# Kernel tuning notes

Hardware: AMD Instinct MI355X
Metric: run time of the kernel (lower is better)

The kernel has to match this reference:

```python
import jax, jax.numpy as jnp
import numpy as np

HID = 256

def setup_inputs() -> dict:
    key = jax.random.key(0)
    ks = jax.random.split(key, 16)
    B, N, DIN, DOUT = 256, 1024, 64, 128
    def lin(k, fin, fout):
        kw, kb = jax.random.split(k)
        s = 1.0 / np.sqrt(fin)
        W = jax.random.uniform(kw, (fin, fout), jnp.float32, -s, s)
        b = jax.random.uniform(kb, (fout,), jnp.float32, -s, s)
        return W, b
    x = jax.random.normal(ks[0], (B, N, DIN), jnp.float32)
    mask = jax.random.randint(ks[1], (B, N), 0, 2) > 0
    pw1, pb1 = lin(ks[2], DIN, HID)
    pw2, pb2 = lin(ks[3], HID, HID)
    pw3, pb3 = lin(ks[4], HID, HID)
    rw1, rb1 = lin(ks[5], HID, HID)
    rw2, rb2 = lin(ks[6], HID, HID)
    rw3, rb3 = lin(ks[7], HID, DOUT)
    return dict(x=x, mask=mask, pw1=pw1, pb1=pb1, pw2=pw2, pb2=pb2, pw3=pw3, pb3=pb3,
                rw1=rw1, rb1=rb1, rw2=rw2, rb2=rb2, rw3=rw3, rb3=rb3)

def reference(x, mask, pw1, pb1, pw2, pb2, pw3, pb3, rw1, rb1, rw2, rb2, rw3, rb3):
    # x: [B, N, din], mask: [B, N] bool
    # phi per element (padding elements are zeroed before the pool, matching
    # the torch pack/pad pipeline which only runs phi on valid elements)
    h = jax.nn.relu(jnp.einsum('bnd,dh->bnh', x, pw1) + pb1)
    h = jax.nn.relu(jnp.einsum('bnh,hk->bnk', h, pw2) + pb2)
    h = jnp.einsum('bnh,hk->bnk', h, pw3) + pb3
    m = mask.astype(x.dtype)[..., None]                  # [B, N, 1]
    pooled = jnp.sum(h * m, axis=1)                      # [B, 256]
    o = jax.nn.relu(pooled @ rw1 + rb1)
    o = jax.nn.relu(o @ rw2 + rb2)
    o = o @ rw3 + rb3                                    # [B, dout]
    # rows with zero valid elements get exactly 0 (torch leaves res at 0.0)
    valid = jnp.any(mask, axis=1, keepdims=True)
    return jnp.where(valid, o, jnp.zeros((), dtype=o.dtype))
```

## Files before the change

kernel.cpp:

```cpp
#include <hip/hip_runtime.h>

namespace {
constexpr int NB = 256, NN = 1024, DIN = 64, HID = 256, DOUT = 128;
constexpr int MT = 64;

typedef __attribute__((ext_vector_type(8))) short bf16x8;
typedef __attribute__((ext_vector_type(4))) float f32x4;

constexpr size_t PW1_OFF = 0;
constexpr size_t PW2_OFF = (size_t)DIN * HID * 2;

__device__ inline unsigned short f2bf(float f) {
    union { float f; unsigned u; } v; v.f = f;
    unsigned r = v.u + 0x7FFF + ((v.u >> 16) & 1);
    return (unsigned short)(r >> 16);
}

__global__ void prep(const float* __restrict__ pw1, const float* __restrict__ pw2,
                     unsigned short* __restrict__ w1p, unsigned short* __restrict__ w2p) {
    int i = blockIdx.x * 256 + threadIdx.x;
    if (i < DIN * HID / 8) {
        int s0 = i * 8;
        int k = s0 >> 8, n0 = s0 & 255;
        float4 v0 = *(const float4*)(pw1 + s0);
        float4 v1 = *(const float4*)(pw1 + s0 + 4);
        float vv[8] = {v0.x, v0.y, v0.z, v0.w, v1.x, v1.y, v1.z, v1.w};
        int j = k & 7, quad = (k >> 3) & 3, kk = k >> 5;
#pragma unroll
        for (int e = 0; e < 8; ++e) {
            int n = n0 + e, strip = n >> 4, l15 = n & 15;
            w1p[strip * 1024 + kk * 512 + (quad * 16 + l15) * 8 + j] = f2bf(vv[e]);
        }
    }
    if (i < HID * HID / 8) {
        int s0 = i * 8;
        int k = s0 >> 8, n0 = s0 & 255;
        float4 v0 = *(const float4*)(pw2 + s0);
        float4 v1 = *(const float4*)(pw2 + s0 + 4);
        float vv[8] = {v0.x, v0.y, v0.z, v0.w, v1.x, v1.y, v1.z, v1.w};
        int j = k & 7, quad = (k >> 3) & 3, kk = k >> 5;
#pragma unroll
        for (int e = 0; e < 8; ++e) {
            int n = n0 + e, strip = n >> 4, l15 = n & 15;
            w2p[strip * 4096 + kk * 512 + (quad * 16 + l15) * 8 + j] = f2bf(vv[e]);
        }
    }
}

__device__ inline float4 dotseg(const float* __restrict__ buf, const float* __restrict__ W,
                                int c, int s) {
    const float4* W4 = (const float4*)W;
    float4 acc = make_float4(0.f, 0.f, 0.f, 0.f);
#pragma unroll 8
    for (int i = 0; i < 32; ++i) {
        int k = s * 32 + i;
        float bk = buf[k];
        float4 w = W4[(size_t)k * 64 + c];
        acc.x = fmaf(bk, w.x, acc.x);
        acc.y = fmaf(bk, w.y, acc.y);
        acc.z = fmaf(bk, w.z, acc.z);
        acc.w = fmaf(bk, w.w, acc.w);
    }
    return acc;
}

__launch_bounds__(512, 2)
__global__ void deepset(const float* __restrict__ x, const int* __restrict__ mask,
                        const float* __restrict__ pb1, const float* __restrict__ pb2,
                        const unsigned short* __restrict__ w1p,
                        const unsigned short* __restrict__ w2p,
                        const float* __restrict__ pw3, const float* __restrict__ pb3,
                        const float* __restrict__ rw1, const float* __restrict__ rb1,
                        const float* __restrict__ rw2, const float* __restrict__ rb2,
                        const float* __restrict__ rw3, const float* __restrict__ rb3,
                        float* __restrict__ out)
{
    __shared__ unsigned short xs[2][MT * 64];
    __shared__ unsigned short h1s[MT * 256];
    __shared__ short vlist[NN];
    __shared__ float pooledS[HID];
    __shared__ float part[8][HID];
    __shared__ float bufB[HID], bufC[HID];
    __shared__ int cnt_s;

    const int b = blockIdx.x, t = threadIdx.x;
    const int lane = t & 63, wq = t >> 6;
    const int quad = lane >> 4, l15 = lane & 15;

    if (t == 0) cnt_s = 0;
    __syncthreads();
    if (mask[b * NN + t] != 0)       { int i = atomicAdd(&cnt_s, 1); vlist[i] = (short)t; }
    if (mask[b * NN + t + 512] != 0) { int i = atomicAdd(&cnt_s, 1); vlist[i] = (short)(t + 512); }
    __syncthreads();
    const int cnt = cnt_s;

    const uint4* w1q = (const uint4*)w1p;
    const uint4* w2q = (const uint4*)w2p;
    uint4 w1f[2][2], w2f[8][2];
#pragma unroll
    for (int j = 0; j < 2; ++j) {
        int strip = wq * 2 + j;
#pragma unroll
        for (int kk = 0; kk < 2; ++kk) w1f[kk][j] = w1q[(strip * 2 + kk) * 64 + lane];
#pragma unroll
        for (int kk = 0; kk < 8; ++kk) w2f[kk][j] = w2q[(strip * 8 + kk) * 64 + lane];
    }
    float bias1[2], bias2[2];
#pragma unroll
    for (int j = 0; j < 2; ++j) {
        int c = wq * 32 + j * 16 + l15;
        bias1[j] = pb1[c]; bias2[j] = pb2[c];
    }

    float pool[2] = {0.f, 0.f};
    const float* xb = x + (size_t)b * NN * DIN;
    const int gr = t >> 3, seg8 = t & 7;
    const int xoff = gr * 64 + ((seg8 ^ (gr & 7)) << 3);

    {
        float4 a0 = make_float4(0.f,0.f,0.f,0.f), a1 = a0;
        if (gr < min(MT, cnt)) {
            const float4* p = (const float4*)(xb + (size_t)vlist[gr] * DIN + seg8 * 8);
            a0 = p[0]; a1 = p[1];
        }
        unsigned short tmp[8] = {f2bf(a0.x),f2bf(a0.y),f2bf(a0.z),f2bf(a0.w),
                                 f2bf(a1.x),f2bf(a1.y),f2bf(a1.z),f2bf(a1.w)};
        *(uint4*)&xs[0][xoff] = *(const uint4*)tmp;
    }

    int cur = 0;
    for (int base = 0; base < cnt; base += MT) {
        __syncthreads();

        f32x4 acc[4][2];
#pragma unroll
        for (int f = 0; f < 4; ++f)
#pragma unroll
            for (int j = 0; j < 2; ++j) acc[f][j] = (f32x4){0.f,0.f,0.f,0.f};
#pragma unroll
        for (int kk = 0; kk < 2; ++kk) {
            bf16x8 a[4];
#pragma unroll
            for (int f = 0; f < 4; ++f)
                a[f] = *(const bf16x8*)&xs[cur][(f*16 + l15)*64 + (((kk*4 + quad) ^ (l15 & 7)) << 3)];
#pragma unroll
            for (int j = 0; j < 2; ++j) {
                bf16x8 bw = __builtin_bit_cast(bf16x8, w1f[kk][j]);
#pragma unroll
                for (int f = 0; f < 4; ++f)
                    acc[f][j] = __builtin_amdgcn_mfma_f32_16x16x32_bf16(a[f], bw, acc[f][j], 0, 0, 0);
            }
        }
#pragma unroll
        for (int f = 0; f < 4; ++f)
#pragma unroll
            for (int j = 0; j < 2; ++j) {
                int col = wq * 32 + j * 16 + l15, kb = col >> 3, cl = col & 7;
#pragma unroll
                for (int r = 0; r < 4; ++r) {
                    int row = f * 16 + quad * 4 + r;
                    float h = fmaxf(acc[f][j][r] + bias1[j], 0.f);
                    h1s[row * 256 + ((kb ^ (row & 7)) << 3) + cl] = f2bf(h);
                }
            }

        float4 n0 = make_float4(0.f,0.f,0.f,0.f), n1 = n0;
        const bool hn = (base + MT) < cnt;
        if (hn && gr < cnt - (base + MT)) {
            const float4* p = (const float4*)(xb + (size_t)vlist[base + MT + gr] * DIN + seg8 * 8);
            n0 = p[0]; n1 = p[1];
        }
        __syncthreads();

        f32x4 acc2[4][2];
#pragma unroll
        for (int f = 0; f < 4; ++f)
#pragma unroll
            for (int j = 0; j < 2; ++j) acc2[f][j] = (f32x4){0.f,0.f,0.f,0.f};
#pragma unroll
        for (int kk = 0; kk < 8; ++kk) {
            bf16x8 a[4];
#pragma unroll
            for (int f = 0; f < 4; ++f)
                a[f] = *(const bf16x8*)&h1s[(f*16 + l15)*256 + (((kk*4 + quad) ^ (l15 & 7)) << 3)];
#pragma unroll
            for (int j = 0; j < 2; ++j) {
                bf16x8 bw = __builtin_bit_cast(bf16x8, w2f[kk][j]);
#pragma unroll
                for (int f = 0; f < 4; ++f)
                    acc2[f][j] = __builtin_amdgcn_mfma_f32_16x16x32_bf16(a[f], bw, acc2[f][j], 0, 0, 0);
            }
        }
#pragma unroll
        for (int f = 0; f < 4; ++f)
#pragma unroll
            for (int r = 0; r < 4; ++r) {
                bool v = (base + f * 16 + quad * 4 + r) < cnt;
#pragma unroll
                for (int j = 0; j < 2; ++j) {
                    float h = fmaxf(acc2[f][j][r] + bias2[j], 0.f);
                    pool[j] += v ? h : 0.f;
                }
            }

        if (hn) {
            unsigned short tmp[8] = {f2bf(n0.x),f2bf(n0.y),f2bf(n0.z),f2bf(n0.w),
                                     f2bf(n1.x),f2bf(n1.y),f2bf(n1.z),f2bf(n1.w)};
            *(uint4*)&xs[cur ^ 1][xoff] = *(const uint4*)tmp;
        }
        cur ^= 1;
    }

#pragma unroll
    for (int j = 0; j < 2; ++j) {
        float v = pool[j];
        v += __shfl_xor(v, 16, 64);
        v += __shfl_xor(v, 32, 64);
        if (quad == 0) pooledS[wq * 32 + j * 16 + l15] = v;
    }
    __syncthreads();

    const int c = t & 63, s = t >> 6;
    {
        float4 p = dotseg(pooledS, pw3, c, s);
        ((float4*)part[s])[c] = p;
        __syncthreads();
        if (t < HID) {
            float v = (float)cnt * pb3[t];
#pragma unroll
            for (int g = 0; g < 8; ++g) v += part[g][t];
            bufB[t] = v;
        }
        __syncthreads();
    }
    {
        float4 p = dotseg(bufB, rw1, c, s);
        ((float4*)part[s])[c] = p;
        __syncthreads();
        if (t < HID) {
            float v = rb1[t];
#pragma unroll
            for (int g = 0; g < 8; ++g) v += part[g][t];
            bufC[t] = fmaxf(v, 0.f);
        }
        __syncthreads();
    }
    {
        float4 p = dotseg(bufC, rw2, c, s);
        ((float4*)part[s])[c] = p;
        __syncthreads();
        if (t < HID) {
            float v = rb2[t];
#pragma unroll
            for (int g = 0; g < 8; ++g) v += part[g][t];
            bufB[t] = fmaxf(v, 0.f);
        }
        __syncthreads();
    }
    {
        const int c4 = t & 31, s4 = t >> 5;
        const float4* W4 = (const float4*)rw3;
        float4 acc = make_float4(0.f, 0.f, 0.f, 0.f);
#pragma unroll 8
        for (int i = 0; i < 16; ++i) {
            int k = s4 * 16 + i;
            float bk = bufB[k];
            float4 w = W4[(size_t)k * 32 + c4];
            acc.x = fmaf(bk, w.x, acc.x);
            acc.y = fmaf(bk, w.y, acc.y);
            acc.z = fmaf(bk, w.z, acc.z);
            acc.w = fmaf(bk, w.w, acc.w);
        }
        float* part2 = &part[0][0];
        ((float4*)(part2 + s4 * DOUT))[c4] = acc;
        __syncthreads();
        if (t < DOUT) {
            float v = rb3[t];
#pragma unroll
            for (int g = 0; g < 16; ++g) v += part2[g * DOUT + t];
            out[b * DOUT + t] = (cnt > 0) ? v : 0.f;
        }
    }
}
}

extern "C" void kernel_launch(void* const* d_in, const int* in_sizes, int n_in,
                              void* d_out, int out_size, void* d_ws, size_t ws_size,
                              hipStream_t stream) {
    const float* x    = (const float*)d_in[0];
    const int*   mask = (const int*)  d_in[1];
    const float* pw1  = (const float*)d_in[2];
    const float* pb1  = (const float*)d_in[3];
    const float* pw2  = (const float*)d_in[4];
    const float* pb2  = (const float*)d_in[5];
    const float* pw3  = (const float*)d_in[6];
    const float* pb3  = (const float*)d_in[7];
    const float* rw1  = (const float*)d_in[8];
    const float* rb1  = (const float*)d_in[9];
    const float* rw2  = (const float*)d_in[10];
    const float* rb2  = (const float*)d_in[11];
    const float* rw3  = (const float*)d_in[12];
    const float* rb3  = (const float*)d_in[13];
    float* out = (float*)d_out;

    unsigned short* w1p = (unsigned short*)((char*)d_ws + PW1_OFF);
    unsigned short* w2p = (unsigned short*)((char*)d_ws + PW2_OFF);

    prep<<<dim3(32), dim3(256), 0, stream>>>(pw1, pw2, w1p, w2p);
    deepset<<<dim3(NB), dim3(512), 0, stream>>>(x, mask, pb1, pb2, w1p, w2p,
                                                pw3, pb3, rw1, rb1, rw2, rb2, rw3, rb3, out);
}
```

Baseline: 146.0 us.

## Split phi across two blocks per batch row and move rho to separate kernel

The fused kernel is split in two. phi_half runs two blocks per batch row, each taking half the set elements with a 32-row tile and higher occupancy, and writes partial pooled sums and counts to workspace. rho_k then sums the partials and runs the rho MLP, with two batch rows per block. The change also compacts the mask with a ballot, swaps the MFMA operand order so outputs are written as packed bf16 stores, and raises MFMA priority with setprio. The aim is to put more blocks on the GPU and shorten each block's serial work, at the cost of an extra launch and a workspace round trip.

```diff
diff --git a/kernel.cpp b/kernel.cpp
--- a/kernel.cpp
+++ b/kernel.cpp
@@ -2,13 +2,16 @@
 
 namespace {
 constexpr int NB = 256, NN = 1024, DIN = 64, HID = 256, DOUT = 128;
-constexpr int MT = 64;
+constexpr int MT = 32;
+constexpr int NH = 512;
 
 typedef __attribute__((ext_vector_type(8))) short bf16x8;
 typedef __attribute__((ext_vector_type(4))) float f32x4;
 
-constexpr size_t PW1_OFF = 0;
-constexpr size_t PW2_OFF = (size_t)DIN * HID * 2;
+constexpr size_t PW1_OFF  = 0;
+constexpr size_t PW2_OFF  = (size_t)DIN * HID * 2;
+constexpr size_t POOL_OFF = PW2_OFF + (size_t)HID * HID * 2;
+constexpr size_t CNT_OFF  = POOL_OFF + (size_t)2 * NB * HID * 4;
 
 __device__ inline unsigned short f2bf(float f) {
     union { float f; unsigned u; } v; v.f = f;
@@ -47,15 +50,192 @@
     }
 }
 
-__device__ inline float4 dotseg(const float* __restrict__ buf, const float* __restrict__ W,
-                                int c, int s) {
+__launch_bounds__(512, 4)
+__global__ void phi_half(const float* __restrict__ x, const int* __restrict__ mask,
+                         const float* __restrict__ pb1, const float* __restrict__ pb2,
+                         const unsigned short* __restrict__ w1p,
+                         const unsigned short* __restrict__ w2p,
+                         float* __restrict__ pool_part, int* __restrict__ cnt_part)
+{
+    __shared__ unsigned short xs[2][MT * 64];
+    __shared__ unsigned short h1s[MT * 256];
+    __shared__ short vlist[NH];
+    __shared__ int cnt_s;
+
+    const int bid = blockIdx.x;
+    const int b = bid >> 1, half = bid & 1;
+    const int t = threadIdx.x;
+    const int lane = t & 63, wq = t >> 6;
+    const int quad = lane >> 4, l15 = lane & 15;
+
+    if (t == 0) cnt_s = 0;
+    __syncthreads();
+    {
+        int m = mask[b * NN + half * NH + t] != 0;
+        unsigned long long bal = __ballot(m);
+        int pos = __popcll(bal & ((1ULL << lane) - 1ULL));
+        int wbase = 0;
+        if (lane == 0) wbase = atomicAdd(&cnt_s, (int)__popcll(bal));
+        wbase = __shfl(wbase, 0, 64);
+        if (m) vlist[wbase + pos] = (short)t;
+    }
+    __syncthreads();
+    const int cnt = cnt_s;
+
+    const uint4* w1q = (const uint4*)w1p;
+    const uint4* w2q = (const uint4*)w2p;
+    uint4 w1f[2][2], w2f[8][2];
+#pragma unroll
+    for (int j = 0; j < 2; ++j) {
+        int strip = wq * 2 + j;
+#pragma unroll
+        for (int kk = 0; kk < 2; ++kk) w1f[kk][j] = w1q[(strip * 2 + kk) * 64 + lane];
+#pragma unroll
+        for (int kk = 0; kk < 8; ++kk) w2f[kk][j] = w2q[(strip * 8 + kk) * 64 + lane];
+    }
+
+    const float* xb = x + ((size_t)b * NN + (size_t)half * NH) * DIN;
+    const int gr = t >> 4, s16 = t & 15;
+    const int xoff = gr * 64 + (((s16 >> 1) ^ (gr & 7)) << 3) + ((s16 & 1) << 2);
+
+    {
+        float4 a0 = make_float4(0.f, 0.f, 0.f, 0.f);
+        if (gr < min(MT, cnt))
+            a0 = *(const float4*)(xb + (size_t)vlist[gr] * DIN + s16 * 4);
+        unsigned lo = (unsigned)f2bf(a0.x) | ((unsigned)f2bf(a0.y) << 16);
+        unsigned hi = (unsigned)f2bf(a0.z) | ((unsigned)f2bf(a0.w) << 16);
+        *(uint2*)&xs[0][xoff] = make_uint2(lo, hi);
+    }
+
+    float pool[2][4] = {{0.f, 0.f, 0.f, 0.f}, {0.f, 0.f, 0.f, 0.f}};
+    const int cb0 = wq * 32 + quad * 4;
+    const int sw = l15 & 7;
+    int cur = 0;
+
+    for (int base = 0; base < cnt; base += MT) {
+        __syncthreads();
+
+        f32x4 acc[2][2];
+#pragma unroll
+        for (int j = 0; j < 2; ++j)
+#pragma unroll
+            for (int f = 0; f < 2; ++f) acc[j][f] = (f32x4){0.f, 0.f, 0.f, 0.f};
+        __builtin_amdgcn_s_setprio(1);
+#pragma unroll
+        for (int kk = 0; kk < 2; ++kk) {
+            bf16x8 a[2];
+#pragma unroll
+            for (int f = 0; f < 2; ++f)
+                a[f] = *(const bf16x8*)&xs[cur][(f * 16 + l15) * 64 + (((kk * 4 + quad) ^ sw) << 3)];
+#pragma unroll
+            for (int j = 0; j < 2; ++j) {
+                bf16x8 bw = __builtin_bit_cast(bf16x8, w1f[kk][j]);
+#pragma unroll
+                for (int f = 0; f < 2; ++f)
+                    acc[j][f] = __builtin_amdgcn_mfma_f32_16x16x32_bf16(bw, a[f], acc[j][f], 0, 0, 0);
+            }
+        }
+        __builtin_amdgcn_s_setprio(0);
+
+#pragma unroll
+        for (int j = 0; j < 2; ++j) {
+            float4 b1 = *(const float4*)&pb1[cb0 + j * 16];
+            int kb = wq * 4 + j * 2 + (quad >> 1);
+#pragma unroll
+            for (int f = 0; f < 2; ++f) {
+                int row = f * 16 + l15;
+                unsigned lo = (unsigned)f2bf(fmaxf(acc[j][f][0] + b1.x, 0.f))
+                            | ((unsigned)f2bf(fmaxf(acc[j][f][1] + b1.y, 0.f)) << 16);
+                unsigned hi = (unsigned)f2bf(fmaxf(acc[j][f][2] + b1.z, 0.f))
+                            | ((unsigned)f2bf(fmaxf(acc[j][f][3] + b1.w, 0.f)) << 16);
+                *(uint2*)&h1s[row * 256 + ((kb ^ sw) << 3) + ((quad & 1) << 2)] = make_uint2(lo, hi);
+            }
+        }
+
+        float4 n0 = make_float4(0.f, 0.f, 0.f, 0.f);
+        const bool hn = (base + MT) < cnt;
+        if (hn && gr < cnt - (base + MT))
+            n0 = *(const float4*)(xb + (size_t)vlist[base + MT + gr] * DIN + s16 * 4);
+
+        __syncthreads();
+
+        f32x4 acc2[2][2];
+#pragma unroll
+        for (int j = 0; j < 2; ++j)
+#pragma unroll
+            for (int f = 0; f < 2; ++f) acc2[j][f] = (f32x4){0.f, 0.f, 0.f, 0.f};
+        __builtin_amdgcn_s_setprio(1);
+#pragma unroll
+        for (int kk = 0; kk < 8; ++kk) {
+            bf16x8 a[2];
+#pragma unroll
+            for (int f = 0; f < 2; ++f)
+                a[f] = *(const bf16x8*)&h1s[(f * 16 + l15) * 256 + (((kk * 4 + quad) ^ sw) << 3)];
+#pragma unroll
+            for (int j = 0; j < 2; ++j) {
+                bf16x8 bw = __builtin_bit_cast(bf16x8, w2f[kk][j]);
+#pragma unroll
+                for (int f = 0; f < 2; ++f)
+                    acc2[j][f] = __builtin_amdgcn_mfma_f32_16x16x32_bf16(bw, a[f], acc2[j][f], 0, 0, 0);
+            }
+        }
+        __builtin_amdgcn_s_setprio(0);
+
+#pragma unroll
+        for (int j = 0; j < 2; ++j) {
+            float4 b2 = *(const float4*)&pb2[cb0 + j * 16];
+#pragma unroll
+            for (int f = 0; f < 2; ++f) {
+                bool vf = (base + f * 16 + l15) < cnt;
+                float h0 = fmaxf(acc2[j][f][0] + b2.x, 0.f);
+                float h1 = fmaxf(acc2[j][f][1] + b2.y, 0.f);
+                float h2 = fmaxf(acc2[j][f][2] + b2.z, 0.f);
+                float h3 = fmaxf(acc2[j][f][3] + b2.w, 0.f);
+                pool[j][0] += vf ? h0 : 0.f;
+                pool[j][1] += vf ? h1 : 0.f;
+                pool[j][2] += vf ? h2 : 0.f;
+                pool[j][3] += vf ? h3 : 0.f;
+            }
+        }
+
+        if (hn) {
+            unsigned lo = (unsigned)f2bf(n0.x) | ((unsigned)f2bf(n0.y) << 16);
+            unsigned hi = (unsigned)f2bf(n0.z) | ((unsigned)f2bf(n0.w) << 16);
+            *(uint2*)&xs[cur ^ 1][xoff] = make_uint2(lo, hi);
+        }
+        cur ^= 1;
+    }
+
+#pragma unroll
+    for (int j = 0; j < 2; ++j)
+#pragma unroll
+        for (int r = 0; r < 4; ++r) {
+            float v = pool[j][r];
+            v += __shfl_xor(v, 1, 64);
+            v += __shfl_xor(v, 2, 64);
+            v += __shfl_xor(v, 4, 64);
+            v += __shfl_xor(v, 8, 64);
+            pool[j][r] = v;
+        }
+    if (l15 == 0) {
+#pragma unroll
+        for (int j = 0; j < 2; ++j) {
+            float4 pv = make_float4(pool[j][0], pool[j][1], pool[j][2], pool[j][3]);
+            *(float4*)&pool_part[(size_t)bid * HID + cb0 + j * 16] = pv;
+        }
+    }
+    if (t == 0) cnt_part[bid] = cnt;
+}
+
+__device__ inline float4 gemvseg(const float* __restrict__ buf, const float* __restrict__ W,
+                                 int c, int s, int nseg, int strid4) {
     const float4* W4 = (const float4*)W;
     float4 acc = make_float4(0.f, 0.f, 0.f, 0.f);
 #pragma unroll 8
-    for (int i = 0; i < 32; ++i) {
-        int k = s * 32 + i;
+    for (int i = 0; i < nseg; ++i) {
+        int k = s * nseg + i;
         float bk = buf[k];
-        float4 w = W4[(size_t)k * 64 + c];
+        float4 w = W4[(size_t)k * strid4 + c];
         acc.x = fmaf(bk, w.x, acc.x);
         acc.y = fmaf(bk, w.y, acc.y);
         acc.z = fmaf(bk, w.z, acc.z);
@@ -64,221 +244,68 @@
     return acc;
 }
 
-__launch_bounds__(512, 2)
-__global__ void deepset(const float* __restrict__ x, const int* __restrict__ mask,
-                        const float* __restrict__ pb1, const float* __restrict__ pb2,
-                        const unsigned short* __restrict__ w1p,
-                        const unsigned short* __restrict__ w2p,
-                        const float* __restrict__ pw3, const float* __restrict__ pb3,
-                        const float* __restrict__ rw1, const float* __restrict__ rb1,
-                        const float* __restrict__ rw2, const float* __restrict__ rb2,
-                        const float* __restrict__ rw3, const float* __restrict__ rb3,
-                        float* __restrict__ out)
+__launch_bounds__(512)
+__global__ void rho_k(const float* __restrict__ pool_part, const int* __restrict__ cnt_part,
+                      const float* __restrict__ pw3, const float* __restrict__ pb3,
+                      const float* __restrict__ rw1, const float* __restrict__ rb1,
+                      const float* __restrict__ rw2, const float* __restrict__ rb2,
+                      const float* __restrict__ rw3, const float* __restrict__ rb3,
+                      float* __restrict__ out)
 {
-    __shared__ unsigned short xs[2][MT * 64];
-    __shared__ unsigned short h1s[MT * 256];
-    __shared__ short vlist[NN];
-    __shared__ float pooledS[HID];
-    __shared__ float part[8][HID];
-    __shared__ float bufB[HID], bufC[HID];
-    __shared__ int cnt_s;
-
-    const int b = blockIdx.x, t = threadIdx.x;
-    const int lane = t & 63, wq = t >> 6;
-    const int quad = lane >> 4, l15 = lane & 15;
-
-    if (t == 0) cnt_s = 0;
+    __shared__ float bufA[2][HID], bufB[2][HID];
+    __shared__ float part[2][4][HID];
+    __shared__ int cnts[2];
+    const int t = threadIdx.x;
+    const int g = t >> 8, gt = t & 255;
+    const int b = blockIdx.x * 2 + g;
+
+    if (gt == 0) cnts[g] = cnt_part[2 * b] + cnt_part[2 * b + 1];
+    bufA[g][gt] = pool_part[(size_t)(2 * b) * HID + gt]
+                + pool_part[(size_t)(2 * b + 1) * HID + gt];
     __syncthreads();
-    if (mask[b * NN + t] != 0)       { int i = atomicAdd(&cnt_s, 1); vlist[i] = (short)t; }
-    if (mask[b * NN + t + 512] != 0) { int i = atomicAdd(&cnt_s, 1); vlist[i] = (short)(t + 512); }
-    __syncthreads();
-    const int cnt = cnt_s;
-
-    const uint4* w1q = (const uint4*)w1p;
-    const uint4* w2q = (const uint4*)w2p;
-    uint4 w1f[2][2], w2f[8][2];
-#pragma unroll
-    for (int j = 0; j < 2; ++j) {
-        int strip = wq * 2 + j;
-#pragma unroll
-        for (int kk = 0; kk < 2; ++kk) w1f[kk][j] = w1q[(strip * 2 + kk) * 64 + lane];
-#pragma unroll
-        for (int kk = 0; kk < 8; ++kk) w2f[kk][j] = w2q[(strip * 8 + kk) * 64 + lane];
-    }
-    float bias1[2], bias2[2];
-#pragma unroll
-    for (int j = 0; j < 2; ++j) {
-        int c = wq * 32 + j * 16 + l15;
-        bias1[j] = pb1[c]; bias2[j] = pb2[c];
-    }
-
-    float pool[2] = {0.f, 0.f};
-    const float* xb = x + (size_t)b * NN * DIN;
-    const int gr = t >> 3, seg8 = t & 7;
-    const int xoff = gr * 64 + ((seg8 ^ (gr & 7)) << 3);
-
-    {
-        float4 a0 = make_float4(0.f,0.f,0.f,0.f), a1 = a0;
-        if (gr < min(MT, cnt)) {
-            const float4* p = (const float4*)(xb + (size_t)vlist[gr] * DIN + seg8 * 8);
-            a0 = p[0]; a1 = p[1];
-        }
-        unsigned short tmp[8] = {f2bf(a0.x),f2bf(a0.y),f2bf(a0.z),f2bf(a0.w),
-                                 f2bf(a1.x),f2bf(a1.y),f2bf(a1.z),f2bf(a1.w)};
-        *(uint4*)&xs[0][xoff] = *(const uint4*)tmp;
-    }
-
-    int cur = 0;
-    for (int base = 0; base < cnt; base += MT) {
-        __syncthreads();
-
-        f32x4 acc[4][2];
-#pragma unroll
-        for (int f = 0; f < 4; ++f)
-#pragma unroll
-            for (int j = 0; j < 2; ++j) acc[f][j] = (f32x4){0.f,0.f,0.f,0.f};
-#pragma unroll
-        for (int kk = 0; kk < 2; ++kk) {
-            bf16x8 a[4];
-#pragma unroll
-            for (int f = 0; f < 4; ++f)
-                a[f] = *(const bf16x8*)&xs[cur][(f*16 + l15)*64 + (((kk*4 + quad) ^ (l15 & 7)) << 3)];
-#pragma unroll
-            for (int j = 0; j < 2; ++j) {
-                bf16x8 bw = __builtin_bit_cast(bf16x8, w1f[kk][j]);
-#pragma unroll
-                for (int f = 0; f < 4; ++f)
-                    acc[f][j] = __builtin_amdgcn_mfma_f32_16x16x32_bf16(a[f], bw, acc[f][j], 0, 0, 0);
-            }
-        }
-#pragma unroll
-        for (int f = 0; f < 4; ++f)
-#pragma unroll
-            for (int j = 0; j < 2; ++j) {
-                int col = wq * 32 + j * 16 + l15, kb = col >> 3, cl = col & 7;
-#pragma unroll
-                for (int r = 0; r < 4; ++r) {
-                    int row = f * 16 + quad * 4 + r;
-                    float h = fmaxf(acc[f][j][r] + bias1[j], 0.f);
-                    h1s[row * 256 + ((kb ^ (row & 7)) << 3) + cl] = f2bf(h);
-                }
-            }
-
-        float4 n0 = make_float4(0.f,0.f,0.f,0.f), n1 = n0;
-        const bool hn = (base + MT) < cnt;
-        if (hn && gr < cnt - (base + MT)) {
-            const float4* p = (const float4*)(xb + (size_t)vlist[base + MT + gr] * DIN + seg8 * 8);
-            n0 = p[0]; n1 = p[1];
-        }
-        __syncthreads();
-
-        f32x4 acc2[4][2];
-#pragma unroll
-        for (int f = 0; f < 4; ++f)
-#pragma unroll
-            for (int j = 0; j < 2; ++j) acc2[f][j] = (f32x4){0.f,0.f,0.f,0.f};
-#pragma unroll
-        for (int kk = 0; kk < 8; ++kk) {
-            bf16x8 a[4];
-#pragma unroll
-            for (int f = 0; f < 4; ++f)
-                a[f] = *(const bf16x8*)&h1s[(f*16 + l15)*256 + (((kk*4 + quad) ^ (l15 & 7)) << 3)];
-#pragma unroll
-            for (int j = 0; j < 2; ++j) {
-                bf16x8 bw = __builtin_bit_cast(bf16x8, w2f[kk][j]);
-#pragma unroll
-                for (int f = 0; f < 4; ++f)
-                    acc2[f][j] = __builtin_amdgcn_mfma_f32_16x16x32_bf16(a[f], bw, acc2[f][j], 0, 0, 0);
-            }
-        }
-#pragma unroll
-        for (int f = 0; f < 4; ++f)
-#pragma unroll
-            for (int r = 0; r < 4; ++r) {
-                bool v = (base + f * 16 + quad * 4 + r) < cnt;
-#pragma unroll
-                for (int j = 0; j < 2; ++j) {
-                    float h = fmaxf(acc2[f][j][r] + bias2[j], 0.f);
-                    pool[j] += v ? h : 0.f;
-                }
-            }
-
-        if (hn) {
-            unsigned short tmp[8] = {f2bf(n0.x),f2bf(n0.y),f2bf(n0.z),f2bf(n0.w),
-                                     f2bf(n1.x),f2bf(n1.y),f2bf(n1.z),f2bf(n1.w)};
-            *(uint4*)&xs[cur ^ 1][xoff] = *(const uint4*)tmp;
-        }
-        cur ^= 1;
-    }
-
-#pragma unroll
-    for (int j = 0; j < 2; ++j) {
-        float v = pool[j];
-        v += __shfl_xor(v, 16, 64);
-        v += __shfl_xor(v, 32, 64);
-        if (quad == 0) pooledS[wq * 32 + j * 16 + l15] = v;
-    }
-    __syncthreads();
-
-    const int c = t & 63, s = t >> 6;
-    {
-        float4 p = dotseg(pooledS, pw3, c, s);
-        ((float4*)part[s])[c] = p;
-        __syncthreads();
-        if (t < HID) {
-            float v = (float)cnt * pb3[t];
-#pragma unroll
-            for (int g = 0; g < 8; ++g) v += part[g][t];
-            bufB[t] = v;
-        }
-        __syncthreads();
-    }
-    {
-        float4 p = dotseg(bufB, rw1, c, s);
-        ((float4*)part[s])[c] = p;
-        __syncthreads();
-        if (t < HID) {
-            float v = rb1[t];
-#pragma unroll
-            for (int g = 0; g < 8; ++g) v += part[g][t];
-            bufC[t] = fmaxf(v, 0.f);
-        }
-        __syncthreads();
-    }
-    {
-        float4 p = dotseg(bufC, rw2, c, s);
-        ((float4*)part[s])[c] = p;
-        __syncthreads();
-        if (t < HID) {
-            float v = rb2[t];
-#pragma unroll
-            for (int g = 0; g < 8; ++g) v += part[g][t];
-            bufB[t] = fmaxf(v, 0.f);
-        }
-        __syncthreads();
-    }
-    {
-        const int c4 = t & 31, s4 = t >> 5;
-        const float4* W4 = (const float4*)rw3;
-        float4 acc = make_float4(0.f, 0.f, 0.f, 0.f);
-#pragma unroll 8
-        for (int i = 0; i < 16; ++i) {
-            int k = s4 * 16 + i;
-            float bk = bufB[k];
-            float4 w = W4[(size_t)k * 32 + c4];
-            acc.x = fmaf(bk, w.x, acc.x);
-            acc.y = fmaf(bk, w.y, acc.y);
-            acc.z = fmaf(bk, w.z, acc.z);
-            acc.w = fmaf(bk, w.w, acc.w);
-        }
-        float* part2 = &part[0][0];
-        ((float4*)(part2 + s4 * DOUT))[c4] = acc;
-        __syncthreads();
-        if (t < DOUT) {
-            float v = rb3[t];
-#pragma unroll
-            for (int g = 0; g < 16; ++g) v += part2[g * DOUT + t];
-            out[b * DOUT + t] = (cnt > 0) ? v : 0.f;
+
+    const int c = gt & 63, s = gt >> 6;
+    {
+        float4 p = gemvseg(bufA[g], pw3, c, s, 64, 64);
+        ((float4*)part[g][s])[c] = p;
+        __syncthreads();
+        float v = (float)cnts[g] * pb3[gt];
+#pragma unroll
+        for (int q = 0; q < 4; ++q) v += part[g][q][gt];
+        bufB[g][gt] = v;
+        __syncthreads();
+    }
+    {
+        float4 p = gemvseg(bufB[g], rw1, c, s, 64, 64);
+        ((float4*)part[g][s])[c] = p;
+        __syncthreads();
+        float v = rb1[gt];
+#pragma unroll
+        for (int q = 0; q < 4; ++q) v += part[g][q][gt];
+        bufA[g][gt] = fmaxf(v, 0.f);
+        __syncthreads();
+    }
+    {
+        float4 p = gemvseg(bufA[g], rw2, c, s, 64, 64);
+        ((float4*)part[g][s])[c] = p;
+        __syncthreads();
+        float v = rb2[gt];
+#pragma unroll
+        for (int q = 0; q < 4; ++q) v += part[g][q][gt];
+        bufB[g][gt] = fmaxf(v, 0.f);
+        __syncthreads();
+    }
+    {
+        const int c4 = gt & 31, s4 = gt >> 5;
+        float4 p = gemvseg(bufB[g], rw3, c4, s4, 32, 32);
+        float* pf = &part[g][0][0];
+        ((float4*)(pf + s4 * DOUT))[c4] = p;
+        __syncthreads();
+        if (gt < DOUT) {
+            float v = rb3[gt];
+#pragma unroll
+            for (int q = 0; q < 8; ++q) v += pf[q * DOUT + gt];
+            out[(size_t)b * DOUT + gt] = (cnts[g] > 0) ? v : 0.f;
         }
     }
 }
@@ -305,8 +332,12 @@
 
     unsigned short* w1p = (unsigned short*)((char*)d_ws + PW1_OFF);
     unsigned short* w2p = (unsigned short*)((char*)d_ws + PW2_OFF);
+    float* pool_part = (float*)((char*)d_ws + POOL_OFF);
+    int* cnt_part = (int*)((char*)d_ws + CNT_OFF);
 
     prep<<<dim3(32), dim3(256), 0, stream>>>(pw1, pw2, w1p, w2p);
-    deepset<<<dim3(NB), dim3(512), 0, stream>>>(x, mask, pb1, pb2, w1p, w2p,
-                                                pw3, pb3, rw1, rb1, rw2, rb2, rw3, rb3, out);
-}
+    phi_half<<<dim3(NB * 2), dim3(512), 0, stream>>>(x, mask, pb1, pb2, w1p, w2p,
+                                                     pool_part, cnt_part);
+    rho_k<<<dim3(NB / 2), dim3(512), 0, stream>>>(pool_part, cnt_part, pw3, pb3,
+                                                  rw1, rb1, rw2, rb2, rw3, rb3, out);
+}
```

Result: slower. 188.9 us (+29.4%).

## Split each batch row across two 512-thread halves in a 1024-thread block

Applied to the files above, without the earlier changes.

Each block now runs 1024 threads, and each half processes its own 512-element slice of the set with its own xs and h1s buffers. The two partial pools are summed before the rho MLP, and that MLP is split over 16 or 32 segments. Compaction now uses a wave ballot plus one atomic per wave instead of per-element atomics. The aim is to halve the serial phi loop per block and raise per-CU parallelism, at the cost of running both halves to the longer half's count and losing the two-blocks-per-CU occupancy.

```diff
diff --git a/kernel.cpp b/kernel.cpp
--- a/kernel.cpp
+++ b/kernel.cpp
@@ -3,12 +3,13 @@
 namespace {
 constexpr int NB = 256, NN = 1024, DIN = 64, HID = 256, DOUT = 128;
 constexpr int MT = 64;
+constexpr int NH2 = 512;
 
 typedef __attribute__((ext_vector_type(8))) short bf16x8;
 typedef __attribute__((ext_vector_type(4))) float f32x4;
 
-constexpr size_t PW1_OFF = 0;
-constexpr size_t PW2_OFF = (size_t)DIN * HID * 2;
+constexpr size_t PW1_OFF  = 0;
+constexpr size_t PW2_OFF  = (size_t)DIN * HID * 2;
 
 __device__ inline unsigned short f2bf(float f) {
     union { float f; unsigned u; } v; v.f = f;
@@ -47,13 +48,13 @@
     }
 }
 
-__device__ inline float4 dotseg(const float* __restrict__ buf, const float* __restrict__ W,
-                                int c, int s) {
+__device__ inline float4 dotseg16(const float* __restrict__ buf, const float* __restrict__ W,
+                                  int c, int s) {
     const float4* W4 = (const float4*)W;
     float4 acc = make_float4(0.f, 0.f, 0.f, 0.f);
 #pragma unroll 8
-    for (int i = 0; i < 32; ++i) {
-        int k = s * 32 + i;
+    for (int i = 0; i < 16; ++i) {
+        int k = s * 16 + i;
         float bk = buf[k];
         float4 w = W4[(size_t)k * 64 + c];
         acc.x = fmaf(bk, w.x, acc.x);
@@ -64,35 +65,45 @@
     return acc;
 }
 
-__launch_bounds__(512, 2)
-__global__ void deepset(const float* __restrict__ x, const int* __restrict__ mask,
-                        const float* __restrict__ pb1, const float* __restrict__ pb2,
-                        const unsigned short* __restrict__ w1p,
-                        const unsigned short* __restrict__ w2p,
-                        const float* __restrict__ pw3, const float* __restrict__ pb3,
-                        const float* __restrict__ rw1, const float* __restrict__ rb1,
-                        const float* __restrict__ rw2, const float* __restrict__ rb2,
-                        const float* __restrict__ rw3, const float* __restrict__ rb3,
-                        float* __restrict__ out)
+__launch_bounds__(1024, 1)
+__global__ void deepset_fused(const float* __restrict__ x, const int* __restrict__ mask,
+                              const float* __restrict__ pb1, const float* __restrict__ pb2,
+                              const unsigned short* __restrict__ w1p,
+                              const unsigned short* __restrict__ w2p,
+                              const float* __restrict__ pw3, const float* __restrict__ pb3,
+                              const float* __restrict__ rw1, const float* __restrict__ rb1,
+                              const float* __restrict__ rw2, const float* __restrict__ rb2,
+                              const float* __restrict__ rw3, const float* __restrict__ rb3,
+                              float* __restrict__ out)
 {
-    __shared__ unsigned short xs[2][MT * 64];
-    __shared__ unsigned short h1s[MT * 256];
-    __shared__ short vlist[NN];
-    __shared__ float pooledS[HID];
-    __shared__ float part[8][HID];
+    __shared__ unsigned short xs[2][2][MT * 64];
+    __shared__ unsigned short h1s[2][MT * 256];
+    __shared__ short vlist[2][NH2];
+    __shared__ float poolH[2][HID];
+    __shared__ float part[16][HID];
     __shared__ float bufB[HID], bufC[HID];
-    __shared__ int cnt_s;
-
-    const int b = blockIdx.x, t = threadIdx.x;
-    const int lane = t & 63, wq = t >> 6;
+    __shared__ int cnt_sh[2];
+
+    const int b = blockIdx.x;
+    const int t = threadIdx.x;
+    const int hh = t >> 9, u = t & 511;
+    const int lane = u & 63, wq = u >> 6;
     const int quad = lane >> 4, l15 = lane & 15;
 
-    if (t == 0) cnt_s = 0;
+    if (t < 2) cnt_sh[t] = 0;
     __syncthreads();
-    if (mask[b * NN + t] != 0)       { int i = atomicAdd(&cnt_s, 1); vlist[i] = (short)t; }
-    if (mask[b * NN + t + 512] != 0) { int i = atomicAdd(&cnt_s, 1); vlist[i] = (short)(t + 512); }
+    {
+        int m = mask[b * NN + hh * NH2 + u] != 0;
+        unsigned long long bal = __ballot(m);
+        int pos = __popcll(bal & ((1ULL << lane) - 1ULL));
+        int wbase = 0;
+        if (lane == 0) wbase = atomicAdd(&cnt_sh[hh], (int)__popcll(bal));
+        wbase = __shfl(wbase, 0, 64);
+        if (m) vlist[hh][wbase + pos] = (short)u;
+    }
     __syncthreads();
-    const int cnt = cnt_s;
+    const int cnt = cnt_sh[hh];
+    const int mx = max(cnt_sh[0], cnt_sh[1]);
 
     const uint4* w1q = (const uint4*)w1p;
     const uint4* w2q = (const uint4*)w2p;
@@ -113,23 +124,23 @@
     }
 
     float pool[2] = {0.f, 0.f};
-    const float* xb = x + (size_t)b * NN * DIN;
-    const int gr = t >> 3, seg8 = t & 7;
+    const float* xb = x + ((size_t)b * NN + (size_t)hh * NH2) * DIN;
+    const int gr = u >> 3, seg8 = u & 7;
     const int xoff = gr * 64 + ((seg8 ^ (gr & 7)) << 3);
 
     {
         float4 a0 = make_float4(0.f,0.f,0.f,0.f), a1 = a0;
         if (gr < min(MT, cnt)) {
-            const float4* p = (const float4*)(xb + (size_t)vlist[gr] * DIN + seg8 * 8);
+            const float4* p = (const float4*)(xb + (size_t)vlist[hh][gr] * DIN + seg8 * 8);
             a0 = p[0]; a1 = p[1];
         }
         unsigned short tmp[8] = {f2bf(a0.x),f2bf(a0.y),f2bf(a0.z),f2bf(a0.w),
                                  f2bf(a1.x),f2bf(a1.y),f2bf(a1.z),f2bf(a1.w)};
-        *(uint4*)&xs[0][xoff] = *(const uint4*)tmp;
+        *(uint4*)&xs[hh][0][xoff] = *(const uint4*)tmp;
     }
 
     int cur = 0;
-    for (int base = 0; base < cnt; base += MT) {
+    for (int base = 0; base < mx; base += MT) {
         __syncthreads();
 
         f32x4 acc[4][2];
@@ -142,7 +153,7 @@
             bf16x8 a[4];
 #pragma unroll
             for (int f = 0; f < 4; ++f)
-                a[f] = *(const bf16x8*)&xs[cur][(f*16 + l15)*64 + (((kk*4 + quad) ^ (l15 & 7)) << 3)];
+                a[f] = *(const bf16x8*)&xs[hh][cur][(f*16 + l15)*64 + (((kk*4 + quad) ^ (l15 & 7)) << 3)];
 #pragma unroll
             for (int j = 0; j < 2; ++j) {
                 bf16x8 bw = __builtin_bit_cast(bf16x8, w1f[kk][j]);
@@ -160,14 +171,14 @@
                 for (int r = 0; r < 4; ++r) {
                     int row = f * 16 + quad * 4 + r;
                     float h = fmaxf(acc[f][j][r] + bias1[j], 0.f);
-                    h1s[row * 256 + ((kb ^ (row & 7)) << 3) + cl] = f2bf(h);
+                    h1s[hh][row * 256 + ((kb ^ (row & 7)) << 3) + cl] = f2bf(h);
                 }
             }
 
         float4 n0 = make_float4(0.f,0.f,0.f,0.f), n1 = n0;
-        const bool hn = (base + MT) < cnt;
-        if (hn && gr < cnt - (base + MT)) {
-            const float4* p = (const float4*)(xb + (size_t)vlist[base + MT + gr] * DIN + seg8 * 8);
+        const bool hstore = (base + MT) < mx;
+        if (gr < cnt - (base + MT)) {
+            const float4* p = (const float4*)(xb + (size_t)vlist[hh][base + MT + gr] * DIN + seg8 * 8);
             n0 = p[0]; n1 = p[1];
         }
         __syncthreads();
@@ -182,7 +193,7 @@
             bf16x8 a[4];
 #pragma unroll
             for (int f = 0; f < 4; ++f)
-                a[f] = *(const bf16x8*)&h1s[(f*16 + l15)*256 + (((kk*4 + quad) ^ (l15 & 7)) << 3)];
+                a[f] = *(const bf16x8*)&h1s[hh][(f*16 + l15)*256 + (((kk*4 + quad) ^ (l15 & 7)) << 3)];
 #pragma unroll
             for (int j = 0; j < 2; ++j) {
                 bf16x8 bw = __builtin_bit_cast(bf16x8, w2f[kk][j]);
@@ -203,10 +214,10 @@
                 }
             }
 
-        if (hn) {
+        if (hstore) {
             unsigned short tmp[8] = {f2bf(n0.x),f2bf(n0.y),f2bf(n0.z),f2bf(n0.w),
                                      f2bf(n1.x),f2bf(n1.y),f2bf(n1.z),f2bf(n1.w)};
-            *(uint4*)&xs[cur ^ 1][xoff] = *(const uint4*)tmp;
+            *(uint4*)&xs[hh][cur ^ 1][xoff] = *(const uint4*)tmp;
         }
         cur ^= 1;
     }
@@ -216,43 +227,47 @@
         float v = pool[j];
         v += __shfl_xor(v, 16, 64);
         v += __shfl_xor(v, 32, 64);
-        if (quad == 0) pooledS[wq * 32 + j * 16 + l15] = v;
+        if (quad == 0) poolH[hh][wq * 32 + j * 16 + l15] = v;
     }
     __syncthreads();
 
+    const int ctot = cnt_sh[0] + cnt_sh[1];
+    if (t < HID) bufC[t] = poolH[0][t] + poolH[1][t];
+    __syncthreads();
+
     const int c = t & 63, s = t >> 6;
     {
-        float4 p = dotseg(pooledS, pw3, c, s);
+        float4 p = dotseg16(bufC, pw3, c, s);
         ((float4*)part[s])[c] = p;
         __syncthreads();
         if (t < HID) {
-            float v = (float)cnt * pb3[t];
-#pragma unroll
-            for (int g = 0; g < 8; ++g) v += part[g][t];
+            float v = (float)ctot * pb3[t];
+#pragma unroll
+            for (int g = 0; g < 16; ++g) v += part[g][t];
             bufB[t] = v;
         }
         __syncthreads();
     }
     {
-        float4 p = dotseg(bufB, rw1, c, s);
+        float4 p = dotseg16(bufB, rw1, c, s);
         ((float4*)part[s])[c] = p;
         __syncthreads();
         if (t < HID) {
             float v = rb1[t];
 #pragma unroll
-            for (int g = 0; g < 8; ++g) v += part[g][t];
+            for (int g = 0; g < 16; ++g) v += part[g][t];
             bufC[t] = fmaxf(v, 0.f);
         }
         __syncthreads();
     }
     {
-        float4 p = dotseg(bufC, rw2, c, s);
+        float4 p = dotseg16(bufC, rw2, c, s);
         ((float4*)part[s])[c] = p;
         __syncthreads();
         if (t < HID) {
             float v = rb2[t];
 #pragma unroll
-            for (int g = 0; g < 8; ++g) v += part[g][t];
+            for (int g = 0; g < 16; ++g) v += part[g][t];
             bufB[t] = fmaxf(v, 0.f);
         }
         __syncthreads();
@@ -262,8 +277,8 @@
         const float4* W4 = (const float4*)rw3;
         float4 acc = make_float4(0.f, 0.f, 0.f, 0.f);
 #pragma unroll 8
-        for (int i = 0; i < 16; ++i) {
-            int k = s4 * 16 + i;
+        for (int i = 0; i < 8; ++i) {
+            int k = s4 * 8 + i;
             float bk = bufB[k];
             float4 w = W4[(size_t)k * 32 + c4];
             acc.x = fmaf(bk, w.x, acc.x);
@@ -277,8 +292,8 @@
         if (t < DOUT) {
             float v = rb3[t];
 #pragma unroll
-            for (int g = 0; g < 16; ++g) v += part2[g * DOUT + t];
-            out[b * DOUT + t] = (cnt > 0) ? v : 0.f;
+            for (int g = 0; g < 32; ++g) v += part2[g * DOUT + t];
+            out[b * DOUT + t] = (ctot > 0) ? v : 0.f;
         }
     }
 }
@@ -307,6 +322,7 @@
     unsigned short* w2p = (unsigned short*)((char*)d_ws + PW2_OFF);
 
     prep<<<dim3(32), dim3(256), 0, stream>>>(pw1, pw2, w1p, w2p);
-    deepset<<<dim3(NB), dim3(512), 0, stream>>>(x, mask, pb1, pb2, w1p, w2p,
-                                                pw3, pb3, rw1, rb1, rw2, rb2, rw3, rb3, out);
-}
+    deepset_fused<<<dim3(NB), dim3(1024), 0, stream>>>(x, mask, pb1, pb2, w1p, w2p,
+                                                       pw3, pb3, rw1, rb1, rw2, rb2, rw3, rb3,
+                                                       out);
+}
```

After: 227.8 us. +56.0%, slower.

## Fuse weight prep into main kernel and software-pipeline layer1/layer2 across tiles

Applied to the files above, without the earlier changes.

Drops the separate prep kernel launch. Each block now loads pw1/pw2 directly with strided fp32 reads and converts them to bf16 fragments in registers. The tile loop is skewed so each iteration computes layer 1 for the next tile and layer 2 for the previous one, using a double-buffered h1 tile in shared memory, which halves the barriers per tile. Mask compaction uses a wave ballot with one atomic per wave. The costs are redundant uncoalesced weight loads in every block, twice the LDS for h1, and launch bounds relaxed to one block per CU, which may reduce occupancy.

```diff
diff --git a/kernel.cpp b/kernel.cpp
--- a/kernel.cpp
+++ b/kernel.cpp
@@ -6,45 +6,11 @@
 
 typedef __attribute__((ext_vector_type(8))) short bf16x8;
 typedef __attribute__((ext_vector_type(4))) float f32x4;
-
-constexpr size_t PW1_OFF = 0;
-constexpr size_t PW2_OFF = (size_t)DIN * HID * 2;
 
 __device__ inline unsigned short f2bf(float f) {
     union { float f; unsigned u; } v; v.f = f;
     unsigned r = v.u + 0x7FFF + ((v.u >> 16) & 1);
     return (unsigned short)(r >> 16);
-}
-
-__global__ void prep(const float* __restrict__ pw1, const float* __restrict__ pw2,
-                     unsigned short* __restrict__ w1p, unsigned short* __restrict__ w2p) {
-    int i = blockIdx.x * 256 + threadIdx.x;
-    if (i < DIN * HID / 8) {
-        int s0 = i * 8;
-        int k = s0 >> 8, n0 = s0 & 255;
-        float4 v0 = *(const float4*)(pw1 + s0);
-        float4 v1 = *(const float4*)(pw1 + s0 + 4);
-        float vv[8] = {v0.x, v0.y, v0.z, v0.w, v1.x, v1.y, v1.z, v1.w};
-        int j = k & 7, quad = (k >> 3) & 3, kk = k >> 5;
-#pragma unroll
-        for (int e = 0; e < 8; ++e) {
-            int n = n0 + e, strip = n >> 4, l15 = n & 15;
-            w1p[strip * 1024 + kk * 512 + (quad * 16 + l15) * 8 + j] = f2bf(vv[e]);
-        }
-    }
-    if (i < HID * HID / 8) {
-        int s0 = i * 8;
-        int k = s0 >> 8, n0 = s0 & 255;
-        float4 v0 = *(const float4*)(pw2 + s0);
-        float4 v1 = *(const float4*)(pw2 + s0 + 4);
-        float vv[8] = {v0.x, v0.y, v0.z, v0.w, v1.x, v1.y, v1.z, v1.w};
-        int j = k & 7, quad = (k >> 3) & 3, kk = k >> 5;
-#pragma unroll
-        for (int e = 0; e < 8; ++e) {
-            int n = n0 + e, strip = n >> 4, l15 = n & 15;
-            w2p[strip * 4096 + kk * 512 + (quad * 16 + l15) * 8 + j] = f2bf(vv[e]);
-        }
-    }
 }
 
 __device__ inline float4 dotseg(const float* __restrict__ buf, const float* __restrict__ W,
@@ -64,11 +30,10 @@
     return acc;
 }
 
-__launch_bounds__(512, 2)
+__launch_bounds__(512, 1)
 __global__ void deepset(const float* __restrict__ x, const int* __restrict__ mask,
-                        const float* __restrict__ pb1, const float* __restrict__ pb2,
-                        const unsigned short* __restrict__ w1p,
-                        const unsigned short* __restrict__ w2p,
+                        const float* __restrict__ pw1, const float* __restrict__ pb1,
+                        const float* __restrict__ pw2, const float* __restrict__ pb2,
                         const float* __restrict__ pw3, const float* __restrict__ pb3,
                         const float* __restrict__ rw1, const float* __restrict__ rb1,
                         const float* __restrict__ rw2, const float* __restrict__ rb2,
@@ -76,7 +41,7 @@
                         float* __restrict__ out)
 {
     __shared__ unsigned short xs[2][MT * 64];
-    __shared__ unsigned short h1s[MT * 256];
+    __shared__ unsigned short h1s[2][MT * 256];
     __shared__ short vlist[NN];
     __shared__ float pooledS[HID];
     __shared__ float part[8][HID];
@@ -89,35 +54,52 @@
 
     if (t == 0) cnt_s = 0;
     __syncthreads();
-    if (mask[b * NN + t] != 0)       { int i = atomicAdd(&cnt_s, 1); vlist[i] = (short)t; }
-    if (mask[b * NN + t + 512] != 0) { int i = atomicAdd(&cnt_s, 1); vlist[i] = (short)(t + 512); }
+#pragma unroll
+    for (int h = 0; h < 2; ++h) {
+        int idx = h * 512 + t;
+        int m = mask[b * NN + idx] != 0;
+        unsigned long long bal = __ballot(m);
+        int pos = __popcll(bal & ((1ULL << lane) - 1ULL));
+        int wbase = 0;
+        if (lane == 0) wbase = atomicAdd(&cnt_s, (int)__popcll(bal));
+        wbase = __shfl(wbase, 0, 64);
+        if (m) vlist[wbase + pos] = (short)idx;
+    }
+
+    uint4 w1f[2][2], w2f[8][2];
+    float bias1[2], bias2[2];
+#pragma unroll
+    for (int j = 0; j < 2; ++j) {
+        const int col = wq * 32 + j * 16 + l15;
+        bias1[j] = pb1[col]; bias2[j] = pb2[col];
+#pragma unroll
+        for (int kk = 0; kk < 2; ++kk) {
+            unsigned short tmp[8];
+#pragma unroll
+            for (int jj = 0; jj < 8; ++jj)
+                tmp[jj] = f2bf(pw1[(size_t)(kk * 32 + quad * 8 + jj) * HID + col]);
+            w1f[kk][j] = *(const uint4*)tmp;
+        }
+#pragma unroll
+        for (int kk = 0; kk < 8; ++kk) {
+            unsigned short tmp[8];
+#pragma unroll
+            for (int jj = 0; jj < 8; ++jj)
+                tmp[jj] = f2bf(pw2[(size_t)(kk * 32 + quad * 8 + jj) * HID + col]);
+            w2f[kk][j] = *(const uint4*)tmp;
+        }
+    }
+
     __syncthreads();
     const int cnt = cnt_s;
-
-    const uint4* w1q = (const uint4*)w1p;
-    const uint4* w2q = (const uint4*)w2p;
-    uint4 w1f[2][2], w2f[8][2];
-#pragma unroll
-    for (int j = 0; j < 2; ++j) {
-        int strip = wq * 2 + j;
-#pragma unroll
-        for (int kk = 0; kk < 2; ++kk) w1f[kk][j] = w1q[(strip * 2 + kk) * 64 + lane];
-#pragma unroll
-        for (int kk = 0; kk < 8; ++kk) w2f[kk][j] = w2q[(strip * 8 + kk) * 64 + lane];
-    }
-    float bias1[2], bias2[2];
-#pragma unroll
-    for (int j = 0; j < 2; ++j) {
-        int c = wq * 32 + j * 16 + l15;
-        bias1[j] = pb1[c]; bias2[j] = pb2[c];
-    }
+    const int T = (cnt + MT - 1) / MT;
 
     float pool[2] = {0.f, 0.f};
     const float* xb = x + (size_t)b * NN * DIN;
     const int gr = t >> 3, seg8 = t & 7;
     const int xoff = gr * 64 + ((seg8 ^ (gr & 7)) << 3);
 
-    {
+    if (T > 0) {
         float4 a0 = make_float4(0.f,0.f,0.f,0.f), a1 = a0;
         if (gr < min(MT, cnt)) {
             const float4* p = (const float4*)(xb + (size_t)vlist[gr] * DIN + seg8 * 8);
@@ -128,87 +110,91 @@
         *(uint4*)&xs[0][xoff] = *(const uint4*)tmp;
     }
 
-    int cur = 0;
-    for (int base = 0; base < cnt; base += MT) {
-        __syncthreads();
-
-        f32x4 acc[4][2];
-#pragma unroll
-        for (int f = 0; f < 4; ++f)
-#pragma unroll
-            for (int j = 0; j < 2; ++j) acc[f][j] = (f32x4){0.f,0.f,0.f,0.f};
-#pragma unroll
-        for (int kk = 0; kk < 2; ++kk) {
-            bf16x8 a[4];
-#pragma unroll
-            for (int f = 0; f < 4; ++f)
-                a[f] = *(const bf16x8*)&xs[cur][(f*16 + l15)*64 + (((kk*4 + quad) ^ (l15 & 7)) << 3)];
-#pragma unroll
-            for (int j = 0; j < 2; ++j) {
-                bf16x8 bw = __builtin_bit_cast(bf16x8, w1f[kk][j]);
+    int p = 0;
+    for (int i = 0; i <= T; ++i, p ^= 1) {
+        __syncthreads();
+        const bool doL1 = (i < T);
+        const bool hn = ((i + 1) * MT) < cnt;
+
+        float4 n0 = make_float4(0.f,0.f,0.f,0.f), n1 = n0;
+        if (doL1 && gr < cnt - (i + 1) * MT) {
+            const float4* pp = (const float4*)(xb + (size_t)vlist[(i + 1) * MT + gr] * DIN + seg8 * 8);
+            n0 = pp[0]; n1 = pp[1];
+        }
+
+        if (doL1) {
+            f32x4 acc[4][2];
+#pragma unroll
+            for (int f = 0; f < 4; ++f)
+#pragma unroll
+                for (int j = 0; j < 2; ++j) acc[f][j] = (f32x4){0.f,0.f,0.f,0.f};
+#pragma unroll
+            for (int kk = 0; kk < 2; ++kk) {
+                bf16x8 a[4];
 #pragma unroll
                 for (int f = 0; f < 4; ++f)
-                    acc[f][j] = __builtin_amdgcn_mfma_f32_16x16x32_bf16(a[f], bw, acc[f][j], 0, 0, 0);
+                    a[f] = *(const bf16x8*)&xs[p][(f*16 + l15)*64 + (((kk*4 + quad) ^ (l15 & 7)) << 3)];
+#pragma unroll
+                for (int j = 0; j < 2; ++j) {
+                    bf16x8 bw = __builtin_bit_cast(bf16x8, w1f[kk][j]);
+#pragma unroll
+                    for (int f = 0; f < 4; ++f)
+                        acc[f][j] = __builtin_amdgcn_mfma_f32_16x16x32_bf16(a[f], bw, acc[f][j], 0, 0, 0);
+                }
             }
-        }
-#pragma unroll
-        for (int f = 0; f < 4; ++f)
-#pragma unroll
-            for (int j = 0; j < 2; ++j) {
-                int col = wq * 32 + j * 16 + l15, kb = col >> 3, cl = col & 7;
+#pragma unroll
+            for (int f = 0; f < 4; ++f)
+#pragma unroll
+                for (int j = 0; j < 2; ++j) {
+                    int col = wq * 32 + j * 16 + l15, kb = col >> 3, cl = col & 7;
+#pragma unroll
+                    for (int r = 0; r < 4; ++r) {
+                        int row = f * 16 + quad * 4 + r;
+                        float h = fmaxf(acc[f][j][r] + bias1[j], 0.f);
+                        h1s[p][row * 256 + ((kb ^ (row & 7)) << 3) + cl] = f2bf(h);
+                    }
+                }
+        }
+
+        if (i > 0) {
+            const int basep = (i - 1) * MT;
+            f32x4 acc2[4][2];
+#pragma unroll
+            for (int f = 0; f < 4; ++f)
+#pragma unroll
+                for (int j = 0; j < 2; ++j) acc2[f][j] = (f32x4){0.f,0.f,0.f,0.f};
+#pragma unroll
+            for (int kk = 0; kk < 8; ++kk) {
+                bf16x8 a[4];
+#pragma unroll
+                for (int f = 0; f < 4; ++f)
+                    a[f] = *(const bf16x8*)&h1s[p ^ 1][(f*16 + l15)*256 + (((kk*4 + quad) ^ (l15 & 7)) << 3)];
+#pragma unroll
+                for (int j = 0; j < 2; ++j) {
+                    bf16x8 bw = __builtin_bit_cast(bf16x8, w2f[kk][j]);
+#pragma unroll
+                    for (int f = 0; f < 4; ++f)
+                        acc2[f][j] = __builtin_amdgcn_mfma_f32_16x16x32_bf16(a[f], bw, acc2[f][j], 0, 0, 0);
+                }
+            }
+#pragma unroll
+            for (int f = 0; f < 4; ++f)
 #pragma unroll
                 for (int r = 0; r < 4; ++r) {
-                    int row = f * 16 + quad * 4 + r;
-                    float h = fmaxf(acc[f][j][r] + bias1[j], 0.f);
-                    h1s[row * 256 + ((kb ^ (row & 7)) << 3) + cl] = f2bf(h);
-                }
-            }
-
-        float4 n0 = make_float4(0.f,0.f,0.f,0.f), n1 = n0;
-        const bool hn = (base + MT) < cnt;
-        if (hn && gr < cnt - (base + MT)) {
-            const float4* p = (const float4*)(xb + (size_t)vlist[base + MT + gr] * DIN + seg8 * 8);
-            n0 = p[0]; n1 = p[1];
-        }
-        __syncthreads();
-
-        f32x4 acc2[4][2];
-#pragma unroll
-        for (int f = 0; f < 4; ++f)
-#pragma unroll
-            for (int j = 0; j < 2; ++j) acc2[f][j] = (f32x4){0.f,0.f,0.f,0.f};
-#pragma unroll
-        for (int kk = 0; kk < 8; ++kk) {
-            bf16x8 a[4];
-#pragma unroll
-            for (int f = 0; f < 4; ++f)
-                a[f] = *(const bf16x8*)&h1s[(f*16 + l15)*256 + (((kk*4 + quad) ^ (l15 & 7)) << 3)];
-#pragma unroll
-            for (int j = 0; j < 2; ++j) {
-                bf16x8 bw = __builtin_bit_cast(bf16x8, w2f[kk][j]);
-#pragma unroll
-                for (int f = 0; f < 4; ++f)
-                    acc2[f][j] = __builtin_amdgcn_mfma_f32_16x16x32_bf16(a[f], bw, acc2[f][j], 0, 0, 0);
-            }
-        }
-#pragma unroll
-        for (int f = 0; f < 4; ++f)
-#pragma unroll
-            for (int r = 0; r < 4; ++r) {
-                bool v = (base + f * 16 + quad * 4 + r) < cnt;
-#pragma unroll
-                for (int j = 0; j < 2; ++j) {
-                    float h = fmaxf(acc2[f][j][r] + bias2[j], 0.f);
-                    pool[j] += v ? h : 0.f;
-                }
-            }
+                    bool v = (basep + f * 16 + quad * 4 + r) < cnt;
+#pragma unroll
+                    for (int j = 0; j < 2; ++j) {
+                        float h = fmaxf(acc2[f][j][r] + bias2[j], 0.f);
+                        pool[j] += v ? h : 0.f;
+                    }
+                }
+        }
 
         if (hn) {
             unsigned short tmp[8] = {f2bf(n0.x),f2bf(n0.y),f2bf(n0.z),f2bf(n0.w),
                                      f2bf(n1.x),f2bf(n1.y),f2bf(n1.z),f2bf(n1.w)};
-            *(uint4*)&xs[cur ^ 1][xoff] = *(const uint4*)tmp;
-        }
-        cur ^= 1;
+            *(uint4*)&xs[p ^ 1][xoff] = *(const uint4*)tmp;
+        }
     }
 
 #pragma unroll
@@ -222,8 +208,8 @@
 
     const int c = t & 63, s = t >> 6;
     {
-        float4 p = dotseg(pooledS, pw3, c, s);
-        ((float4*)part[s])[c] = p;
+        float4 pt = dotseg(pooledS, pw3, c, s);
+        ((float4*)part[s])[c] = pt;
         __syncthreads();
         if (t < HID) {
             float v = (float)cnt * pb3[t];
@@ -234,8 +220,8 @@
         __syncthreads();
     }
     {
-        float4 p = dotseg(bufB, rw1, c, s);
-        ((float4*)part[s])[c] = p;
+        float4 pt = dotseg(bufB, rw1, c, s);
+        ((float4*)part[s])[c] = pt;
         __syncthreads();
         if (t < HID) {
             float v = rb1[t];
@@ -246,8 +232,8 @@
         __syncthreads();
     }
     {
-        float4 p = dotseg(bufC, rw2, c, s);
-        ((float4*)part[s])[c] = p;
+        float4 pt = dotseg(bufC, rw2, c, s);
+        ((float4*)part[s])[c] = pt;
         __syncthreads();
         if (t < HID) {
             float v = rb2[t];
@@ -302,11 +288,8 @@
     const float* rw3  = (const float*)d_in[12];
     const float* rb3  = (const float*)d_in[13];
     float* out = (float*)d_out;
-
-    unsigned short* w1p = (unsigned short*)((char*)d_ws + PW1_OFF);
-    unsigned short* w2p = (unsigned short*)((char*)d_ws + PW2_OFF);
-
-    prep<<<dim3(32), dim3(256), 0, stream>>>(pw1, pw2, w1p, w2p);
-    deepset<<<dim3(NB), dim3(512), 0, stream>>>(x, mask, pb1, pb2, w1p, w2p,
+    (void)d_ws; (void)ws_size;
+
+    deepset<<<dim3(NB), dim3(512), 0, stream>>>(x, mask, pw1, pb1, pw2, pb2,
                                                 pw3, pb3, rw1, rb1, rw2, rb2, rw3, rb3, out);
 }
```

After: 147.7 us. No clear change (+1.2%).
